# Optimization experiments

Hardware: AMD Instinct MI355X
Metric: run time of the kernel (lower is better)

The kernel has to match this reference:

```python
import jax, jax.numpy as jnp
import numpy as np

N = 300000
IN_C = 64
OUT_C = 128
N_Z = 8
B, H, W = 4, 256, 256


def setup_inputs() -> dict:
    key = jax.random.key(0)
    k = jax.random.split(key, 7)
    std = 1.0 / np.sqrt(IN_C)
    return {
        "features": jax.random.normal(k[0], (N, IN_C), dtype=jnp.float32),
        "kernel": jax.random.uniform(k[1], (N_Z, IN_C, OUT_C), dtype=jnp.float32, minval=-std, maxval=std),
        "bias": jnp.zeros((1, OUT_C), dtype=jnp.float32),
        "batch_idx": jax.random.randint(k[2], (N,), 0, B, dtype=jnp.int32),
        "d0_idx": jax.random.randint(k[3], (N,), 0, H, dtype=jnp.int32),
        "d1_idx": jax.random.randint(k[4], (N,), 0, W, dtype=jnp.int32),
        "z_idx": jax.random.randint(k[5], (N,), 0, N_Z, dtype=jnp.int32),
    }


def reference(features, kernel, bias, batch_idx, d0_idx, d1_idx, z_idx):
    # stride s = 1 on the drcv path, so //s is identity
    z = jnp.clip(z_idx, 0, N_Z - 1)
    flat_bev = batch_idx * (H * W) + d0_idx * W + d1_idx  # [N]
    # per-point learned matmul: features[n] @ kernel[z[n]]
    # (computed as a small fixed loop over n_z height bins to avoid
    #  materializing the [N, in_c, out_c] gathered kernel)
    bev_feat = jnp.zeros((features.shape[0], OUT_C), dtype=features.dtype)
    for zz in range(N_Z):
        bev_feat = bev_feat + jnp.where((z == zz)[:, None], features @ kernel[zz], 0.0)
    bev_feat = bev_feat + bias
    # scatter_add into dense BEV
    bev = jnp.zeros((B * H * W, OUT_C), dtype=features.dtype).at[flat_bev].add(bev_feat)
    return bev.reshape(B, H, W, OUT_C).transpose(0, 3, 1, 2)
```

## Files before the change

kernel.cpp:

```cpp
#include <hip/hip_runtime.h>

#define PPB   128
#define NZ    8
#define INC   64
#define OUTC  128
#define NB    4
#define HH    256
#define WWD   256
#define HWD   (HH * WWD)
#define NSEG  (NB * HH)
#define NCELL (NB * HH * WWD)

typedef __attribute__((ext_vector_type(8))) short bf16x8;
typedef __attribute__((ext_vector_type(4))) float f32x4;

__device__ __forceinline__ unsigned bf16_rne(float x) {
    unsigned u = __float_as_uint(x);
    return (u + 0x7FFFu + ((u >> 16) & 1u)) >> 16;
}
__device__ __forceinline__ unsigned pack2(float lo, float hi) {
    return bf16_rne(lo) | (bf16_rne(hi) << 16);
}

__global__ __launch_bounds__(256) void wprep_kernel(const float* __restrict__ kw,
                                                    unsigned short* __restrict__ wt) {
    int z = blockIdx.x;
    const float* src = kw + (size_t)z * INC * OUTC;
    unsigned short* dst = wt + (size_t)z * OUTC * INC;
    int t = threadIdx.x;
    for (int c = t; c < OUTC; c += 256) {
#pragma unroll
        for (int k = 0; k < INC; k += 2) {
            float a = src[(size_t)k * OUTC + c];
            float b = src[(size_t)(k + 1) * OUTC + c];
            *(unsigned*)&dst[(size_t)c * INC + k] = pack2(a, b);
        }
    }
}

__global__ void hist_kernel(const int* __restrict__ z_idx, const int* __restrict__ batch_idx,
                            const int* __restrict__ d0_idx, const int* __restrict__ d1_idx,
                            int* __restrict__ counts, int* __restrict__ cellhist, int n) {
    __shared__ int lc[NZ];
    int t = threadIdx.x;
    if (t < NZ) lc[t] = 0;
    __syncthreads();
    int i = blockIdx.x * blockDim.x + t;
    if (i < n) {
        int z = z_idx[i]; z = z < 0 ? 0 : (z > NZ - 1 ? NZ - 1 : z);
        atomicAdd(&lc[z], 1);
        int cell = (batch_idx[i] * HH + d0_idx[i]) * WWD + d1_idx[i];
        atomicAdd(&cellhist[cell], 1);
    }
    __syncthreads();
    if (t < NZ && lc[t] > 0) atomicAdd(&counts[t], lc[t]);
}

__global__ __launch_bounds__(256) void scan_local(const int* __restrict__ cellhist,
                                                  int* __restrict__ cellstart,
                                                  int* __restrict__ chunksum,
                                                  const int* __restrict__ counts,
                                                  int* __restrict__ pstart) {
    if (blockIdx.x == 0 && threadIdx.x == 0) {
        int off = 0;
        for (int z = 0; z < NZ; ++z) {
            pstart[z] = off;
            off += ((counts[z] + PPB - 1) / PPB) * PPB;
        }
        pstart[NZ] = off;
    }
    __shared__ int ts[256];
    int t = threadIdx.x;
    int base = blockIdx.x * 1024 + t * 4;
    int4 v = *(const int4*)&cellhist[base];
    int s = v.x + v.y + v.z + v.w;
    ts[t] = s;
    __syncthreads();
    for (int d = 1; d < 256; d <<= 1) {
        int x = (t >= d) ? ts[t - d] : 0;
        __syncthreads();
        ts[t] += x;
        __syncthreads();
    }
    int excl = ts[t] - s;
    int4 o;
    o.x = excl; o.y = excl + v.x; o.z = o.y + v.y; o.w = o.z + v.z;
    *(int4*)&cellstart[base] = o;
    if (t == 255) chunksum[blockIdx.x] = ts[255];
}

__global__ __launch_bounds__(256) void scan_add2(int* __restrict__ cellstart,
                                                 const int* __restrict__ chunksum) {
    __shared__ int ts[256];
    int t = threadIdx.x;
    int b = blockIdx.x;
    ts[t] = (t < b) ? chunksum[t] : 0;
    __syncthreads();
    for (int d = 128; d > 0; d >>= 1) {
        if (t < d) ts[t] += ts[t + d];
        __syncthreads();
    }
    int off = ts[0];
    if (off == 0) return;
    int base = b * 1024 + t * 4;
    int4 v = *(int4*)&cellstart[base];
    v.x += off; v.y += off; v.z += off; v.w += off;
    *(int4*)&cellstart[base] = v;
}

__global__ void scatter_kernel(const int* __restrict__ z_idx, const int* __restrict__ batch_idx,
                               const int* __restrict__ d0_idx, const int* __restrict__ d1_idx,
                               const int* __restrict__ pstart, int* __restrict__ cursors,
                               int* __restrict__ cellstart,
                               int* __restrict__ bins, int* __restrict__ segpos, int n) {
    __shared__ int lc[NZ];
    __shared__ int lbase[NZ];
    int t = threadIdx.x;
    if (t < NZ) lc[t] = 0;
    __syncthreads();
    int i = blockIdx.x * blockDim.x + t;
    int z = 0, rank = 0;
    bool valid = (i < n);
    if (valid) {
        z = z_idx[i]; z = z < 0 ? 0 : (z > NZ - 1 ? NZ - 1 : z);
        rank = atomicAdd(&lc[z], 1);
    }
    __syncthreads();
    if (t < NZ) lbase[t] = (lc[t] > 0) ? atomicAdd(&cursors[t], lc[t]) : 0;
    __syncthreads();
    if (valid) {
        int slot = pstart[z] + lbase[z] + rank;
        bins[slot] = i;
        int cell = (batch_idx[i] * HH + d0_idx[i]) * WWD + d1_idx[i];
        int r2 = atomicAdd(&cellstart[cell], 1);
        segpos[slot] = 1 + r2;
    }
}

__global__ __launch_bounds__(256) void gemm_kernel(
        const float* __restrict__ features, const unsigned short* __restrict__ wt,
        const float* __restrict__ bias, const int* __restrict__ counts,
        const int* __restrict__ pstart, const int* __restrict__ bins,
        const int* __restrict__ segpos, unsigned* __restrict__ bevf) {
    __shared__ __align__(16) char lbuf[32768];
    __shared__ int psl[PPB];
    char* Abf = lbuf;
    char* Wbf = lbuf + 16384;

    int start = blockIdx.x * PPB;
    int total = pstart[NZ];
    if (start >= total) return;
    int z = 0;
#pragma unroll
    for (int zz = 1; zz < NZ; ++zz)
        if (start >= pstart[zz]) z = zz;
    int limit = pstart[z] + counts[z] - start;
    if (limit <= 0) return;

    int tid = threadIdx.x;
    if (tid < PPB) psl[tid] = (tid < limit) ? segpos[start + tid] : 0;

    {
        int r = tid >> 1, half = tid & 1;
        int raw = (r < limit) ? bins[start + r] : 0;
        int nid = raw < 0 ? 0 : raw;
        const float4* fp = (const float4*)(features + (size_t)nid * INC) + half * 8;
        float4 f[8];
#pragma unroll
        for (int q = 0; q < 8; ++q) f[q] = fp[q];
        unsigned u[16];
#pragma unroll
        for (int m = 0; m < 8; ++m) {
            u[2 * m]     = pack2(f[m].x, f[m].y);
            u[2 * m + 1] = pack2(f[m].z, f[m].w);
        }
#pragma unroll
        for (int ch = 0; ch < 4; ++ch) {
            int off = (r * 128 + half * 64 + ch * 16) ^ ((r & 7) << 4);
            uint4 val = make_uint4(u[4 * ch], u[4 * ch + 1], u[4 * ch + 2], u[4 * ch + 3]);
            *(uint4*)(Abf + off) = val;
        }
    }
    {
        const uint4* src = (const uint4*)(wt + (size_t)z * OUTC * INC);
#pragma unroll
        for (int i = 0; i < 4; ++i) {
            int s = tid + 256 * i;
            int c = s >> 3, ch = s & 7;
            int off = (c * 128 + ch * 16) ^ ((c & 7) << 4);
            *(uint4*)(Wbf + off) = src[s];
        }
    }
    __syncthreads();

    int wv_ = tid >> 6, l = tid & 63;
    int wr = wv_ >> 1, wc = wv_ & 1;

    f32x4 acc[4][4];
#pragma unroll
    for (int i = 0; i < 4; ++i)
#pragma unroll
        for (int j = 0; j < 4; ++j) acc[i][j] = (f32x4){0.f, 0.f, 0.f, 0.f};

#pragma unroll
    for (int kc = 0; kc < 2; ++kc) {
        bf16x8 af[4], bfr[4];
#pragma unroll
        for (int pb = 0; pb < 4; ++pb) {
            int p = wr * 64 + pb * 16 + (l & 15);
            int off = (p * 128 + kc * 64 + (l >> 4) * 16) ^ ((p & 7) << 4);
            af[pb] = *(const bf16x8*)(Abf + off);
        }
#pragma unroll
        for (int cb = 0; cb < 4; ++cb) {
            int c = wc * 64 + cb * 16 + (l & 15);
            int off = (c * 128 + kc * 64 + (l >> 4) * 16) ^ ((c & 7) << 4);
            bfr[cb] = *(const bf16x8*)(Wbf + off);
        }
#pragma unroll
        for (int pb = 0; pb < 4; ++pb)
#pragma unroll
            for (int cb = 0; cb < 4; ++cb)
                acc[pb][cb] = __builtin_amdgcn_mfma_f32_16x16x32_bf16(
                    af[pb], bfr[cb], acc[pb][cb], 0, 0, 0);
    }
    __syncthreads();

    float bias_c[4];
#pragma unroll
    for (int cb = 0; cb < 4; ++cb) bias_c[cb] = bias[wc * 64 + cb * 16 + (l & 15)];

#pragma unroll
    for (int pb = 0; pb < 4; ++pb) {
#pragma unroll
        for (int cb = 0; cb < 4; ++cb) {
            int c = wc * 64 + cb * 16 + (l & 15);
#pragma unroll
            for (int q = 0; q < 4; ++q) {
                int prow = wr * 64 + pb * 16 + (l >> 4) * 4 + q;
                float v = acc[pb][cb][q] + bias_c[cb];
                int byteoff = (prow * 256 + c * 2) ^ (((prow >> 2) & 3) << 5);
                *(unsigned short*)(lbuf + byteoff) = (unsigned short)bf16_rne(v);
            }
        }
    }
    __syncthreads();

#pragma unroll
    for (int j = 0; j < 8; ++j) {
        int s = j * 256 + tid;
        int prow = s >> 4, chunk = s & 15;
        int byteoff = (prow * 256 + chunk * 16) ^ (((prow >> 2) & 3) << 5);
        uint4 val = *(const uint4*)(lbuf + byteoff);
        int pos = psl[prow];
        *((uint4*)(bevf + (size_t)pos * 64) + chunk) = val;
    }
}

__global__ __launch_bounds__(512) void reduce_kernel(
        const unsigned* __restrict__ bevf, const int* __restrict__ cellstart,
        float* __restrict__ out) {
    __shared__ unsigned tile[256 * 64];
    int t = threadIdx.x;
    int blk = blockIdx.x;
    blk = (blk & 7) * (NSEG / 8) + (blk >> 3);
    int seg = blk;
    int wv = t >> 6, l = t & 63;

    int cell0 = seg * WWD + wv * 32;
    int idx = cell0 + l - 1;
    int bound = 0;
    if (l <= 32) bound = (idx < 0) ? 0 : cellstart[idx];
    int r0 = __shfl(bound, 0);
    int r1 = __shfl(bound, 32);

    int j = 0;
    int ce = __shfl(bound, 1);
    float f0 = 0.f, f1 = 0.f;
    for (int r = r0; r < r1; r += 4) {
        unsigned v[4];
#pragma unroll
        for (int u = 0; u < 4; ++u) {
            int rr = (r + u < r1) ? r + u : r1 - 1;
            v[u] = bevf[(size_t)(rr + 1) * 64 + l];
        }
#pragma unroll
        for (int u = 0; u < 4; ++u) {
            if (r + u >= r1) break;
            while (r + u >= ce) {
                int w = wv * 32 + j;
                tile[w * 64 + ((l + w + (w >> 2)) & 63)] = pack2(f0, f1);
                f0 = 0.f; f1 = 0.f;
                ++j;
                ce = __shfl(bound, j + 1);
            }
            f0 += __uint_as_float(v[u] << 16);
            f1 += __uint_as_float(v[u] & 0xFFFF0000u);
        }
    }
    while (j < 32) {
        int w = wv * 32 + j;
        tile[w * 64 + ((l + w + (w >> 2)) & 63)] = pack2(f0, f1);
        f0 = 0.f; f1 = 0.f;
        ++j;
    }
    __syncthreads();

    int b = seg >> 8, h = seg & 255;
    float* ob = out + (size_t)b * OUTC * HWD + (size_t)h * WWD;
#pragma unroll
    for (int r = 0; r < 16; ++r) {
        int c = wv + 8 * r;
        int d = c >> 1;
        bool hi = c & 1;
        unsigned v0 = tile[(4 * l + 0) * 64 + ((d + 5 * l + 0) & 63)];
        unsigned v1 = tile[(4 * l + 1) * 64 + ((d + 5 * l + 1) & 63)];
        unsigned v2 = tile[(4 * l + 2) * 64 + ((d + 5 * l + 2) & 63)];
        unsigned v3 = tile[(4 * l + 3) * 64 + ((d + 5 * l + 3) & 63)];
        float4 o;
        o.x = __uint_as_float(hi ? (v0 & 0xFFFF0000u) : (v0 << 16));
        o.y = __uint_as_float(hi ? (v1 & 0xFFFF0000u) : (v1 << 16));
        o.z = __uint_as_float(hi ? (v2 & 0xFFFF0000u) : (v2 << 16));
        o.w = __uint_as_float(hi ? (v3 & 0xFFFF0000u) : (v3 << 16));
        *(float4*)(ob + (size_t)c * HWD + 4 * l) = o;
    }
}

__global__ __launch_bounds__(256) void naive_kernel(
        const float* __restrict__ features, const float* __restrict__ kw,
        const float* __restrict__ bias,
        const int* __restrict__ bidx, const int* __restrict__ d0,
        const int* __restrict__ d1, const int* __restrict__ zi,
        float* __restrict__ out, int n) {
    long long gid = (long long)blockIdx.x * blockDim.x + threadIdx.x;
    int pid = (int)(gid >> 7);
    int c   = (int)(gid & (OUTC - 1));
    if (pid >= n) return;
    int z = zi[pid]; z = z < 0 ? 0 : (z > NZ - 1 ? NZ - 1 : z);
    const float4* fp = (const float4*)(features + (size_t)pid * INC);
    const float* wp = kw + (size_t)z * INC * OUTC + c;
    float a0 = bias[c], a1 = 0.f, a2 = 0.f, a3 = 0.f;
#pragma unroll
    for (int i = 0; i < INC / 4; ++i) {
        float4 f = fp[i];
        a0 += f.x * wp[(size_t)(4 * i + 0) * OUTC];
        a1 += f.y * wp[(size_t)(4 * i + 1) * OUTC];
        a2 += f.z * wp[(size_t)(4 * i + 2) * OUTC];
        a3 += f.w * wp[(size_t)(4 * i + 3) * OUTC];
    }
    float acc = (a0 + a1) + (a2 + a3);
    size_t oidx = ((size_t)bidx[pid] * OUTC + c) * HWD + (size_t)d0[pid] * WWD + d1[pid];
    unsafeAtomicAdd(&out[oidx], acc);
}

extern "C" void kernel_launch(void* const* d_in, const int* in_sizes, int n_in,
                              void* d_out, int out_size, void* d_ws, size_t ws_size,
                              hipStream_t stream) {
    const float* features = (const float*)d_in[0];
    const float* kw       = (const float*)d_in[1];
    const float* bias     = (const float*)d_in[2];
    const int* batch_idx  = (const int*)d_in[3];
    const int* d0_idx     = (const int*)d_in[4];
    const int* d1_idx     = (const int*)d_in[5];
    const int* z_idx      = (const int*)d_in[6];
    float* out = (float*)d_out;
    int n = in_sizes[0] / INC;

    size_t binsElems = (size_t)n + (size_t)NZ * PPB;
    size_t bevfBytes = (binsElems + 1) * OUTC * 2;
    size_t wtOff     = (bevfBytes + 255) & ~(size_t)255;
    size_t metaOff   = wtOff + (size_t)NZ * OUTC * INC * 2;
    size_t chOff     = (metaOff + 32 * 4 + 255) & ~(size_t)255;
    size_t csOff     = chOff + (size_t)NCELL * 4;
    size_t ckOff     = csOff + (size_t)(NCELL + 4) * 4;
    size_t binsOff   = (ckOff + 256 * 4 + 255) & ~(size_t)255;
    size_t posOff    = binsOff + binsElems * 4;
    size_t need      = posOff + binsElems * 4 + 16;

    if (ws_size >= need) {
        char* ws = (char*)d_ws;
        unsigned* bevf = (unsigned*)ws;
        unsigned short* wt = (unsigned short*)(ws + wtOff);
        int* meta      = (int*)(ws + metaOff);
        int* counts    = meta;
        int* cursors   = meta + 8;
        int* pstart    = meta + 16;
        int* cellhist  = (int*)(ws + chOff);
        int* cellstart = (int*)(ws + csOff);
        int* chunksum  = (int*)(ws + ckOff);
        int* bins      = (int*)(ws + binsOff);
        int* segpos    = (int*)(ws + posOff);

        hipMemsetAsync(meta, 0, 32 * 4, stream);
        hipMemsetAsync(cellhist, 0, (size_t)NCELL * 4, stream);

        int gb = (n + 255) / 256;
        wprep_kernel<<<NZ, 256, 0, stream>>>(kw, wt);
        hist_kernel<<<gb, 256, 0, stream>>>(z_idx, batch_idx, d0_idx, d1_idx,
                                            counts, cellhist, n);
        scan_local<<<256, 256, 0, stream>>>(cellhist, cellstart, chunksum,
                                            counts, pstart);
        scan_add2<<<256, 256, 0, stream>>>(cellstart, chunksum);
        scatter_kernel<<<gb, 256, 0, stream>>>(z_idx, batch_idx, d0_idx, d1_idx,
                                               pstart, cursors, cellstart,
                                               bins, segpos, n);

        int nblk = (int)((binsElems + PPB - 1) / PPB) + 1;
        gemm_kernel<<<nblk, 256, 0, stream>>>(features, wt, bias, counts, pstart,
                                              bins, segpos, bevf);

        reduce_kernel<<<NSEG, 512, 0, stream>>>(bevf, cellstart, out);
    } else {
        hipMemsetAsync(out, 0, (size_t)out_size * sizeof(float), stream);
        long long threads = (long long)n * OUTC;
        int gb = (int)((threads + 255) / 256);
        naive_kernel<<<gb, 256, 0, stream>>>(features, kw, bias, batch_idx, d0_idx,
                                             d1_idx, z_idx, out, n);
    }
}
```

Measured before the change: 152.5 us.

## Fold workspace memsets into wprep and vectorize reduce with 16-lane cell groups

The two memset calls that cleared the metadata and the per-cell histogram are removed, and the weight-prep kernel now zeroes both buffers itself, saving two stream operations. The reduce kernel is reorganised so that each 16-lane group handles 8 cells, with every lane loading a uint4 (8 bf16 channels) per row instead of one 32-bit word. This gives wider, fewer global loads and shorter serial walks over each cell's rows. The cost is more registers per thread, four LDS stores per cell flush, and a histogram clear that depends on exactly 8 blocks of 256 threads covering NCELL.

Result: faster. 146.7 us (-3.8%).

```diff
diff --git a/kernel.cpp b/kernel.cpp
--- a/kernel.cpp
+++ b/kernel.cpp
@@ -23,11 +23,21 @@
 }
 
 __global__ __launch_bounds__(256) void wprep_kernel(const float* __restrict__ kw,
-                                                    unsigned short* __restrict__ wt) {
+                                                    unsigned short* __restrict__ wt,
+                                                    int* __restrict__ meta,
+                                                    int* __restrict__ cellhist) {
     int z = blockIdx.x;
+    int t = threadIdx.x;
+    if (z == 0 && t < 32) meta[t] = 0;
+    {
+        int4 zero4 = make_int4(0, 0, 0, 0);
+        int4* ch4 = (int4*)cellhist;
+        int idx0 = (z * 256 + t) * 32;
+#pragma unroll
+        for (int i = 0; i < 32; ++i) ch4[idx0 + i] = zero4;
+    }
     const float* src = kw + (size_t)z * INC * OUTC;
     unsigned short* dst = wt + (size_t)z * OUTC * INC;
-    int t = threadIdx.x;
     for (int c = t; c < OUTC; c += 256) {
 #pragma unroll
         for (int k = 0; k < INC; k += 2) {
@@ -265,47 +275,70 @@
     int blk = blockIdx.x;
     blk = (blk & 7) * (NSEG / 8) + (blk >> 3);
     int seg = blk;
-    int wv = t >> 6, l = t & 63;
-
-    int cell0 = seg * WWD + wv * 32;
-    int idx = cell0 + l - 1;
+
+    int qw = t >> 4;
+    int m  = t & 15;
+    int w0 = qw * 8;
+    int cell0 = seg * WWD + w0;
+
+    int idx = cell0 + m - 1;
     int bound = 0;
-    if (l <= 32) bound = (idx < 0) ? 0 : cellstart[idx];
-    int r0 = __shfl(bound, 0);
-    int r1 = __shfl(bound, 32);
-
+    if (m <= 8) bound = (idx < 0) ? 0 : cellstart[idx];
+    int r0 = __shfl(bound, 0, 16);
+    int r1 = __shfl(bound, 8, 16);
+
+    float f[8];
+#pragma unroll
+    for (int i = 0; i < 8; ++i) f[i] = 0.f;
     int j = 0;
-    int ce = __shfl(bound, 1);
-    float f0 = 0.f, f1 = 0.f;
+    int ce = __shfl(bound, 1, 16);
+
     for (int r = r0; r < r1; r += 4) {
-        unsigned v[4];
+        uint4 v[4];
 #pragma unroll
         for (int u = 0; u < 4; ++u) {
             int rr = (r + u < r1) ? r + u : r1 - 1;
-            v[u] = bevf[(size_t)(rr + 1) * 64 + l];
+            v[u] = *(const uint4*)&bevf[(size_t)(rr + 1) * 64 + 4 * m];
         }
 #pragma unroll
         for (int u = 0; u < 4; ++u) {
             if (r + u >= r1) break;
             while (r + u >= ce) {
-                int w = wv * 32 + j;
-                tile[w * 64 + ((l + w + (w >> 2)) & 63)] = pack2(f0, f1);
-                f0 = 0.f; f1 = 0.f;
+                int w = w0 + j;
+                int sb = w + (w >> 2);
+                tile[w * 64 + ((4 * m + 0 + sb) & 63)] = pack2(f[0], f[1]);
+                tile[w * 64 + ((4 * m + 1 + sb) & 63)] = pack2(f[2], f[3]);
+                tile[w * 64 + ((4 * m + 2 + sb) & 63)] = pack2(f[4], f[5]);
+                tile[w * 64 + ((4 * m + 3 + sb) & 63)] = pack2(f[6], f[7]);
+#pragma unroll
+                for (int i = 0; i < 8; ++i) f[i] = 0.f;
                 ++j;
-                ce = __shfl(bound, j + 1);
+                ce = __shfl(bound, j + 1, 16);
             }
-            f0 += __uint_as_float(v[u] << 16);
-            f1 += __uint_as_float(v[u] & 0xFFFF0000u);
-        }
-    }
-    while (j < 32) {
-        int w = wv * 32 + j;
-        tile[w * 64 + ((l + w + (w >> 2)) & 63)] = pack2(f0, f1);
-        f0 = 0.f; f1 = 0.f;
+            f[0] += __uint_as_float(v[u].x << 16);
+            f[1] += __uint_as_float(v[u].x & 0xFFFF0000u);
+            f[2] += __uint_as_float(v[u].y << 16);
+            f[3] += __uint_as_float(v[u].y & 0xFFFF0000u);
+            f[4] += __uint_as_float(v[u].z << 16);
+            f[5] += __uint_as_float(v[u].z & 0xFFFF0000u);
+            f[6] += __uint_as_float(v[u].w << 16);
+            f[7] += __uint_as_float(v[u].w & 0xFFFF0000u);
+        }
+    }
+    while (j < 8) {
+        int w = w0 + j;
+        int sb = w + (w >> 2);
+        tile[w * 64 + ((4 * m + 0 + sb) & 63)] = pack2(f[0], f[1]);
+        tile[w * 64 + ((4 * m + 1 + sb) & 63)] = pack2(f[2], f[3]);
+        tile[w * 64 + ((4 * m + 2 + sb) & 63)] = pack2(f[4], f[5]);
+        tile[w * 64 + ((4 * m + 3 + sb) & 63)] = pack2(f[6], f[7]);
+#pragma unroll
+        for (int i = 0; i < 8; ++i) f[i] = 0.f;
         ++j;
     }
     __syncthreads();
 
+    int wv = t >> 6, l = t & 63;
     int b = seg >> 8, h = seg & 255;
     float* ob = out + (size_t)b * OUTC * HWD + (size_t)h * WWD;
 #pragma unroll
@@ -391,11 +424,8 @@
         int* bins      = (int*)(ws + binsOff);
         int* segpos    = (int*)(ws + posOff);
 
-        hipMemsetAsync(meta, 0, 32 * 4, stream);
-        hipMemsetAsync(cellhist, 0, (size_t)NCELL * 4, stream);
-
         int gb = (n + 255) / 256;
-        wprep_kernel<<<NZ, 256, 0, stream>>>(kw, wt);
+        wprep_kernel<<<NZ, 256, 0, stream>>>(kw, wt, meta, cellhist);
         hist_kernel<<<gb, 256, 0, stream>>>(z_idx, batch_idx, d0_idx, d1_idx,
                                             counts, cellhist, n);
         scan_local<<<256, 256, 0, stream>>>(cellhist, cellstart, chunksum,
```
